# Kernel optimization log

Measured on AMD Instinct MI355X. Metric: run time of the kernel, lower is better.

Reference implementation:

```python
import jax, jax.numpy as jnp
import numpy as np

B, T, D = 4, 1024, 2048
H = 32
HD = D // H  # 64
NEG = -1e9


def setup_inputs() -> dict:
    key = jax.random.key(0)
    ks = jax.random.split(key, 12)
    s = 0.02
    x = jax.random.normal(ks[0], (B, T, D), dtype=jnp.float32)
    # additive causal mask [1, 1, T, T]
    causal = jnp.tril(jnp.ones((T, T), dtype=bool))
    attention_mask = jnp.where(causal, 0.0, NEG).astype(jnp.float32)[None, None]
    cache = jnp.zeros((B, 2, T, H, HD), dtype=jnp.float32)
    return {
        "x": x,
        "attention_mask": attention_mask,
        "cache": cache,
        "cache_update_index": 0,
        "Wq": jax.random.normal(ks[1], (D, D), jnp.float32) * s,
        "bq": jnp.zeros((D,), jnp.float32),
        "Wk": jax.random.normal(ks[2], (D, D), jnp.float32) * s,
        "bk": jnp.zeros((D,), jnp.float32),
        "Wv": jax.random.normal(ks[3], (D, D), jnp.float32) * s,
        "bv": jnp.zeros((D,), jnp.float32),
        "Wo": jax.random.normal(ks[4], (D, D), jnp.float32) * s,
        "bo": jnp.zeros((D,), jnp.float32),
    }


def _split_heads(t):
    b, s, _ = t.shape
    return t.reshape(b, s, H, HD).transpose(0, 2, 1, 3)  # (B,H,T,HD)


def reference(x, attention_mask, cache, cache_update_index, Wq, bq, Wk, bk, Wv, bv, Wo, bo):
    q = _split_heads(x @ Wq + bq)  # (B,H,T,HD)
    k = _split_heads(x @ Wk + bk)
    v = _split_heads(x @ Wv + bv)

    # update KV cache (cache layout: [B, 2, max_len, H, HD])
    k_for_cache = k.transpose(0, 2, 1, 3)  # (B,T,H,HD)
    v_for_cache = v.transpose(0, 2, 1, 3)
    idx = (0, cache_update_index, 0, 0)
    k_cache = jax.lax.dynamic_update_slice(cache[:, 0], k_for_cache, idx)
    v_cache = jax.lax.dynamic_update_slice(cache[:, 1], v_for_cache, idx)
    new_cache = jnp.stack([k_cache, v_cache], axis=1)
    k = k_cache.transpose(0, 2, 1, 3)  # (B,H,S,HD)
    v = v_cache.transpose(0, 2, 1, 3)

    scale = jnp.asarray(HD, q.dtype) ** -0.5
    scores = jnp.einsum("bhqd,bhkd->bhqk", q, k) * scale + attention_mask.astype(q.dtype)
    attn = jax.nn.softmax(scores, axis=-1)
    ctx = jnp.einsum("bhqk,bhkd->bhqd", attn, v)  # (B,H,T,HD)
    merged = ctx.transpose(0, 2, 1, 3).reshape(x.shape[0], x.shape[1], D)
    out = merged @ Wo + bo
    return out, new_cache
```

## Files before the change

### kernel.cpp

```cpp
#include <hip/hip_runtime.h>
#include <hip/hip_bf16.h>
#include <stdint.h>


typedef __hip_bfloat16 bf16;
typedef unsigned short us;
typedef short s16x8 __attribute__((ext_vector_type(8)));
typedef float f32x4 __attribute__((ext_vector_type(4)));

#define T_SEQ   1024
#define D_MODEL 2048

__device__ inline us f2b(float f) {
    bf16 h = __float2bfloat16(f);
    return *(us*)&h;
}

typedef __attribute__((address_space(1))) const void gas_void;
typedef __attribute__((address_space(3))) void las_void;

__device__ inline void gl2lds16(const void* g, void* l) {
    __builtin_amdgcn_global_load_lds((gas_void*)g, (las_void*)l, 16, 0, 0);
}

__global__ __launch_bounds__(256)
void cvtx_kernel(const float* __restrict__ x, us* __restrict__ xb)
{
    const size_t i = ((size_t)blockIdx.x * 256 + threadIdx.x) * 8;
    float4 a = *(const float4*)(x + i);
    float4 b = *(const float4*)(x + i + 4);
    union { uint4 u; us s[8]; } p;
    p.s[0] = f2b(a.x); p.s[1] = f2b(a.y); p.s[2] = f2b(a.z); p.s[3] = f2b(a.w);
    p.s[4] = f2b(b.x); p.s[5] = f2b(b.y); p.s[6] = f2b(b.z); p.s[7] = f2b(b.w);
    *(uint4*)(xb + i) = p.u;
}

__global__ __launch_bounds__(256)
void wtrans_kernel(const float* __restrict__ W0, const float* __restrict__ W1,
                   const float* __restrict__ W2, us* __restrict__ Wt)
{
    __shared__ float tile[64][65];
    const int z = blockIdx.z;
    const float* W = (z == 0) ? W0 : (z == 1) ? W1 : W2;
    us* dst = Wt + (size_t)z * D_MODEL * D_MODEL;

    const int tid = threadIdx.x;
    const int k0 = blockIdx.y * 64, n0 = blockIdx.x * 64;

    const int rr = tid >> 4, cc = (tid & 15) * 4;
    #pragma unroll
    for (int i = 0; i < 4; ++i) {
        float4 v = *(const float4*)(W + (size_t)(k0 + rr + i * 16) * D_MODEL + n0 + cc);
        tile[rr + i * 16][cc]     = v.x;
        tile[rr + i * 16][cc + 1] = v.y;
        tile[rr + i * 16][cc + 2] = v.z;
        tile[rr + i * 16][cc + 3] = v.w;
    }
    __syncthreads();

    const int nr = tid >> 3, kc = (tid & 7) * 8;
    #pragma unroll
    for (int i = 0; i < 2; ++i) {
        const int n = nr + i * 32;
        union { uint4 u; us s[8]; } p;
        #pragma unroll
        for (int j = 0; j < 8; ++j) p.s[j] = f2b(tile[kc + j][n]);
        *(uint4*)(dst + (size_t)(n0 + n) * D_MODEL + k0 + kc) = p.u;
    }
}

template<int MODE>
__global__ __launch_bounds__(256, 3)
void gemm128_kernel(const us* __restrict__ A, const us* __restrict__ Bt,
                    const float* __restrict__ b0, const float* __restrict__ b1,
                    const float* __restrict__ b2,
                    float* __restrict__ out0, float* __restrict__ out1,
                    const int* __restrict__ idxp)
{
    __shared__ __align__(16) us As[128 * 64];
    __shared__ __align__(16) us Bs[128 * 64];

    const int tid  = threadIdx.x;
    const int wv   = tid >> 6;
    const int lane = tid & 63;
    const int quad = lane >> 4;
    const int l15  = lane & 15;
    const int wm   = wv >> 1;
    const int wn   = wv & 1;

    const int gx  = gridDim.x;
    const int nwg = gx * gridDim.y;
    int bid = blockIdx.y * gx + blockIdx.x;
    bid = (bid & 7) * (nwg >> 3) + (bid >> 3);
    const int m0 = (bid / gx) * 128;
    const int n0 = (bid % gx) * 128;

    const int srow = lane >> 3;
    const int scol = ((lane & 7) ^ srow) * 8;
    const us* aG = A  + (size_t)(m0 + wv * 32 + srow) * D_MODEL + scol;
    const us* bG = Bt + (size_t)(n0 + wv * 32 + srow) * D_MODEL + scol;
    us* aL = As + wv * 32 * 64;
    us* bL = Bs + wv * 32 * 64;

    f32x4 acc[4][4];
    #pragma unroll
    for (int mi = 0; mi < 4; ++mi)
        #pragma unroll
        for (int ni = 0; ni < 4; ++ni) acc[mi][ni] = f32x4{0.f, 0.f, 0.f, 0.f};

    const int xr = l15 & 7;
    #define LDA(MI, KK) (*(const s16x8*)(As + (wm * 64 + (MI) * 16 + l15) * 64 \
                          + ((((KK) * 4 + quad) ^ xr) * 8)))
    #define LDB(NI, KK) (*(const s16x8*)(Bs + (wn * 64 + (NI) * 16 + l15) * 64 \
                          + ((((KK) * 4 + quad) ^ xr) * 8)))

    for (int k0 = 0; k0 < D_MODEL; k0 += 64) {
        #pragma unroll
        for (int g = 0; g < 4; ++g) {
            gl2lds16(aG + k0 + g * 8 * D_MODEL, aL + g * 512);
            gl2lds16(bG + k0 + g * 8 * D_MODEL, bL + g * 512);
        }
        __syncthreads();

        #pragma unroll
        for (int kk = 0; kk < 2; ++kk) {
            s16x8 af[4], bfr[4];
            #pragma unroll
            for (int mi = 0; mi < 4; ++mi) af[mi] = LDA(mi, kk);
            #pragma unroll
            for (int ni = 0; ni < 4; ++ni) bfr[ni] = LDB(ni, kk);
            #pragma unroll
            for (int mi = 0; mi < 4; ++mi)
                #pragma unroll
                for (int ni = 0; ni < 4; ++ni)
                    acc[mi][ni] = __builtin_amdgcn_mfma_f32_16x16x32_bf16(
                        af[mi], bfr[ni], acc[mi][ni], 0, 0, 0);
        }
        __syncthreads();
    }
    #undef LDA
    #undef LDB

    const int seg = (MODE == 3) ? (n0 >> 11) : 0;
    const float* bias = (MODE == 3) ? (seg == 0 ? b0 : (seg == 1 ? b1 : b2)) : b0;
    const int idx = (MODE == 3 && seg > 0) ? idxp[0] : 0;

    #pragma unroll
    for (int ni = 0; ni < 4; ++ni) {
        const int col = n0 + wn * 64 + ni * 16 + l15;
        const int cl  = col & (D_MODEL - 1);
        const float bv = bias[cl];
        #pragma unroll
        for (int mi = 0; mi < 4; ++mi) {
            #pragma unroll
            for (int r = 0; r < 4; ++r) {
                const int m = m0 + wm * 64 + mi * 16 + quad * 4 + r;
                const float v = acc[mi][ni][r] + bv;
                if (MODE == 0) {
                    out0[(size_t)m * D_MODEL + cl] = v;
                } else {
                    if (seg == 0) {
                        ((us*)out0)[(size_t)m * D_MODEL + cl] = f2b(v * 0.125f);
                    } else {
                        const int b  = m >> 10;
                        const int tt = ((m & 1023) + idx) & 1023;
                        out1[((size_t)(b * 2 + (seg - 1)) * T_SEQ + tt) * D_MODEL + cl] = v;
                    }
                }
            }
        }
    }
}

#define LDW  72
#define LDWV 70

__global__ __launch_bounds__(512, 4)
void attn_mfma_kernel(const us* __restrict__ q, const float* __restrict__ cache,
                      us* __restrict__ ctx)
{
    __shared__ __align__(16) us Qs[128 * LDW];
    __shared__ __align__(16) us Ks[64 * LDW];
    __shared__ __align__(16) us Vt[64 * LDWV];

    const int tid  = threadIdx.x;
    const int wave = tid >> 6;
    const int lane = tid & 63;
    const int quad = lane >> 4;
    const int l15  = lane & 15;

    const int bh = blockIdx.x;
    const int b  = bh >> 5;
    const int h  = bh & 31;
    const int qt = 7 - blockIdx.y;

    const float* kbase = cache + ((size_t)(b * 2 + 0) * T_SEQ) * D_MODEL + h * 64;
    const float* vbase = cache + ((size_t)(b * 2 + 1) * T_SEQ) * D_MODEL + h * 64;

    {
        const int qrow = tid >> 2;
        const int qp   = tid & 3;
        const uint4* qg = (const uint4*)(q + (size_t)(b * T_SEQ + qt * 128 + qrow) * D_MODEL
                                           + h * 64 + qp * 16);
        uint4 q0 = qg[0], q1 = qg[1];
        *(uint4*)(Qs + qrow * LDW + qp * 16)     = q0;
        *(uint4*)(Qs + qrow * LDW + qp * 16 + 8) = q1;
    }
    __syncthreads();

    const s16x8 qf0 = *(const s16x8*)(Qs + (wave * 16 + l15) * LDW + quad * 8);
    const s16x8 qf1 = *(const s16x8*)(Qs + (wave * 16 + l15) * LDW + 32 + quad * 8);

    f32x4 oacc[4];
    #pragma unroll
    for (int t = 0; t < 4; ++t) oacc[t] = f32x4{0.f, 0.f, 0.f, 0.f};
    float m_run[4] = {-1e30f, -1e30f, -1e30f, -1e30f};
    float l_run[4] = {0.f, 0.f, 0.f, 0.f};

    const int nkt = 2 * qt + 2;

    const int ksrow = tid >> 3;
    const int kp8   = tid & 7;
    const int vs    = tid >> 4;
    const int vp4   = tid & 15;

    for (int kt = 0; kt < nkt; ++kt) {
        __syncthreads();

        {
            const float4* kg = (const float4*)(kbase + (size_t)(kt * 64 + ksrow) * D_MODEL + kp8 * 8);
            float4 k0 = kg[0], k1 = kg[1];
            union { uint4 u; us s[8]; } p;
            p.s[0] = f2b(k0.x); p.s[1] = f2b(k0.y); p.s[2] = f2b(k0.z); p.s[3] = f2b(k0.w);
            p.s[4] = f2b(k1.x); p.s[5] = f2b(k1.y); p.s[6] = f2b(k1.z); p.s[7] = f2b(k1.w);
            *(uint4*)(Ks + ksrow * LDW + kp8 * 8) = p.u;
        }
        {
            const float4 a = *(const float4*)(vbase + (size_t)(kt * 64 + 2 * vs) * D_MODEL + vp4 * 4);
            const float4 c = *(const float4*)(vbase + (size_t)(kt * 64 + 2 * vs + 1) * D_MODEL + vp4 * 4);
            const float av[4] = {a.x, a.y, a.z, a.w};
            const float cv[4] = {c.x, c.y, c.z, c.w};
            #pragma unroll
            for (int j = 0; j < 4; ++j) {
                ushort2 w; w.x = f2b(av[j]); w.y = f2b(cv[j]);
                *(ushort2*)(Vt + (vp4 * 4 + j) * LDWV + 2 * vs) = w;
            }
        }
        __syncthreads();

        const int kbr = kt * 64 - qt * 128;
        if (kbr < wave * 16 + 16) {
            f32x4 sacc[4];
            #pragma unroll
            for (int t = 0; t < 4; ++t) sacc[t] = f32x4{0.f, 0.f, 0.f, 0.f};
            #pragma unroll
            for (int t = 0; t < 4; ++t) {
                s16x8 kf0 = *(const s16x8*)(Ks + (t * 16 + l15) * LDW + quad * 8);
                s16x8 kf1 = *(const s16x8*)(Ks + (t * 16 + l15) * LDW + 32 + quad * 8);
                sacc[t] = __builtin_amdgcn_mfma_f32_16x16x32_bf16(qf0, kf0, sacc[t], 0, 0, 0);
                sacc[t] = __builtin_amdgcn_mfma_f32_16x16x32_bf16(qf1, kf1, sacc[t], 0, 0, 0);
            }

            if (kbr + 63 > wave * 16) {
                #pragma unroll
                for (int t = 0; t < 4; ++t) {
                    const int keyl = kbr + t * 16 + l15;
                    #pragma unroll
                    for (int r = 0; r < 4; ++r) {
                        if (keyl > wave * 16 + quad * 4 + r) sacc[t][r] = -1e30f;
                    }
                }
            }

            float rmax[4];
            #pragma unroll
            for (int r = 0; r < 4; ++r)
                rmax[r] = fmaxf(fmaxf(sacc[0][r], sacc[1][r]), fmaxf(sacc[2][r], sacc[3][r]));
            #pragma unroll
            for (int off = 1; off < 16; off <<= 1) {
                #pragma unroll
                for (int r = 0; r < 4; ++r) rmax[r] = fmaxf(rmax[r], __shfl_xor(rmax[r], off, 16));
            }
            float alpha[4];
            #pragma unroll
            for (int r = 0; r < 4; ++r) {
                const float mnew = fmaxf(m_run[r], rmax[r]);
                alpha[r] = __expf(m_run[r] - mnew);
                m_run[r] = mnew;
            }
            float rsum[4] = {0.f, 0.f, 0.f, 0.f};
            #pragma unroll
            for (int t = 0; t < 4; ++t) {
                #pragma unroll
                for (int r = 0; r < 4; ++r) {
                    const float p = __expf(sacc[t][r] - m_run[r]);
                    sacc[t][r] = p;
                    rsum[r] += p;
                }
            }
            #pragma unroll
            for (int off = 1; off < 16; off <<= 1) {
                #pragma unroll
                for (int r = 0; r < 4; ++r) rsum[r] += __shfl_xor(rsum[r], off, 16);
            }
            #pragma unroll
            for (int r = 0; r < 4; ++r) l_run[r] = l_run[r] * alpha[r] + rsum[r];
            #pragma unroll
            for (int t = 0; t < 4; ++t) {
                #pragma unroll
                for (int r = 0; r < 4; ++r) oacc[t][r] *= alpha[r];
            }

            #pragma unroll
            for (int t = 0; t < 4; ++t) {
                #pragma unroll
                for (int r = 0; r < 4; ++r)
                    Qs[(wave * 16 + quad * 4 + r) * LDW + t * 16 + l15] = f2b(sacc[t][r]);
            }

            s16x8 pf0 = *(const s16x8*)(Qs + (wave * 16 + l15) * LDW + quad * 8);
            s16x8 pf1 = *(const s16x8*)(Qs + (wave * 16 + l15) * LDW + 32 + quad * 8);
            #pragma unroll
            for (int t = 0; t < 4; ++t) {
                s16x8 vf0 = *(const s16x8*)(Vt + (t * 16 + l15) * LDWV + quad * 8);
                s16x8 vf1 = *(const s16x8*)(Vt + (t * 16 + l15) * LDWV + 32 + quad * 8);
                oacc[t] = __builtin_amdgcn_mfma_f32_16x16x32_bf16(pf0, vf0, oacc[t], 0, 0, 0);
                oacc[t] = __builtin_amdgcn_mfma_f32_16x16x32_bf16(pf1, vf1, oacc[t], 0, 0, 0);
            }
        }
    }

    float invl[4];
    #pragma unroll
    for (int r = 0; r < 4; ++r) invl[r] = 1.0f / l_run[r];
    #pragma unroll
    for (int r = 0; r < 4; ++r) {
        const int qrow = qt * 128 + wave * 16 + quad * 4 + r;
        us* orow = ctx + (size_t)(b * T_SEQ + qrow) * D_MODEL + h * 64;
        #pragma unroll
        for (int t = 0; t < 4; ++t) orow[t * 16 + l15] = f2b(oacc[t][r] * invl[r]);
    }
}

extern "C" void kernel_launch(void* const* d_in, const int* in_sizes, int n_in,
                              void* d_out, int out_size, void* d_ws, size_t ws_size,
                              hipStream_t stream)
{
    const float* x    = (const float*)d_in[0];
    const int*   idxp = (const int*)d_in[3];
    const float* Wq   = (const float*)d_in[4];
    const float* bq   = (const float*)d_in[5];
    const float* Wk   = (const float*)d_in[6];
    const float* bk   = (const float*)d_in[7];
    const float* Wv   = (const float*)d_in[8];
    const float* bv   = (const float*)d_in[9];
    const float* Wo   = (const float*)d_in[10];
    const float* bo   = (const float*)d_in[11];

    float* out      = (float*)d_out;
    us*    xb       = (us*)d_out;
    us*    qb       = (us*)d_out + (size_t)8 * 1024 * 1024;
    float* cacheOut = out + (size_t)4 * T_SEQ * D_MODEL;

    us* WT3  = (us*)d_ws;
    us* WTo  = (us*)d_ws;
    us* ctxb = (us*)d_ws + (size_t)4 * 1024 * 1024;

    const dim3 tb(256);

    cvtx_kernel<<<dim3(4096), tb, 0, stream>>>(x, xb);
    wtrans_kernel<<<dim3(32, 32, 3), tb, 0, stream>>>(Wq, Wk, Wv, WT3);

    gemm128_kernel<3><<<dim3(48, 32), tb, 0, stream>>>(
        xb, WT3, bq, bk, bv, (float*)qb, cacheOut, idxp);

    wtrans_kernel<<<dim3(32, 32, 1), tb, 0, stream>>>(Wo, Wo, Wo, WTo);

    attn_mfma_kernel<<<dim3(128, 8), dim3(512), 0, stream>>>(qb, cacheOut, ctxb);

    gemm128_kernel<0><<<dim3(16, 32), tb, 0, stream>>>(
        ctxb, WTo, bo, nullptr, nullptr, out, nullptr, nullptr);
}
```

Measured before the change: 439.0 us.

## Split V projection to emit pre-transposed bf16 V and double-buffer attention K/V tiles

```diff
diff --git a/kernel.cpp b/kernel.cpp
--- a/kernel.cpp
+++ b/kernel.cpp
@@ -37,11 +37,11 @@
 
 __global__ __launch_bounds__(256)
 void wtrans_kernel(const float* __restrict__ W0, const float* __restrict__ W1,
-                   const float* __restrict__ W2, us* __restrict__ Wt)
+                   us* __restrict__ Wt)
 {
     __shared__ float tile[64][65];
     const int z = blockIdx.z;
-    const float* W = (z == 0) ? W0 : (z == 1) ? W1 : W2;
+    const float* W = (z == 0) ? W0 : W1;
     us* dst = Wt + (size_t)z * D_MODEL * D_MODEL;
 
     const int tid = threadIdx.x;
@@ -73,9 +73,8 @@
 __global__ __launch_bounds__(256, 3)
 void gemm128_kernel(const us* __restrict__ A, const us* __restrict__ Bt,
                     const float* __restrict__ b0, const float* __restrict__ b1,
-                    const float* __restrict__ b2,
                     float* __restrict__ out0, float* __restrict__ out1,
-                    const int* __restrict__ idxp)
+                    us* __restrict__ vbt, const int* __restrict__ idxp)
 {
     __shared__ __align__(16) us As[128 * 64];
     __shared__ __align__(16) us Bs[128 * 64];
@@ -141,9 +140,9 @@
     #undef LDA
     #undef LDB
 
-    const int seg = (MODE == 3) ? (n0 >> 11) : 0;
-    const float* bias = (MODE == 3) ? (seg == 0 ? b0 : (seg == 1 ? b1 : b2)) : b0;
-    const int idx = (MODE == 3 && seg > 0) ? idxp[0] : 0;
+    const int seg = (MODE == 4) ? (n0 >> 11) : 0;
+    const float* bias = (MODE == 4) ? (seg == 0 ? b0 : b1) : b0;
+    const int idx = (MODE == 0) ? 0 : idxp[0];
 
     #pragma unroll
     for (int ni = 0; ni < 4; ++ni) {
@@ -152,42 +151,57 @@
         const float bv = bias[cl];
         #pragma unroll
         for (int mi = 0; mi < 4; ++mi) {
+            float vv[4];
             #pragma unroll
             for (int r = 0; r < 4; ++r) {
                 const int m = m0 + wm * 64 + mi * 16 + quad * 4 + r;
                 const float v = acc[mi][ni][r] + bv;
                 if (MODE == 0) {
                     out0[(size_t)m * D_MODEL + cl] = v;
-                } else {
+                } else if (MODE == 4) {
                     if (seg == 0) {
                         ((us*)out0)[(size_t)m * D_MODEL + cl] = f2b(v * 0.125f);
                     } else {
                         const int b  = m >> 10;
                         const int tt = ((m & 1023) + idx) & 1023;
-                        out1[((size_t)(b * 2 + (seg - 1)) * T_SEQ + tt) * D_MODEL + cl] = v;
+                        out1[((size_t)(b * 2 + 0) * T_SEQ + tt) * D_MODEL + cl] = v;
                     }
+                } else {
+                    const int b  = m >> 10;
+                    const int tt = ((m & 1023) + idx) & 1023;
+                    out1[((size_t)(b * 2 + 1) * T_SEQ + tt) * D_MODEL + cl] = v;
+                    vv[r] = v;
                 }
             }
-        }
-    }
-}
-
-#define LDW  72
-#define LDWV 70
+            if (MODE == 5) {
+                const int tok0 = m0 + wm * 64 + mi * 16 + quad * 4;
+                const int bb = tok0 >> 10, t0 = tok0 & 1023;
+                const int hh = cl >> 6, dd = cl & 63;
+                ushort4 pv;
+                pv.x = f2b(vv[0]); pv.y = f2b(vv[1]);
+                pv.z = f2b(vv[2]); pv.w = f2b(vv[3]);
+                *(ushort4*)(vbt + (size_t)((bb * 32 + hh) * 64 + dd) * 1024 + t0) = pv;
+            }
+        }
+    }
+}
+
+#define LDW 72
 
 __global__ __launch_bounds__(512, 4)
 void attn_mfma_kernel(const us* __restrict__ q, const float* __restrict__ cache,
-                      us* __restrict__ ctx)
+                      const us* __restrict__ vbt, us* __restrict__ ctx)
 {
     __shared__ __align__(16) us Qs[128 * LDW];
-    __shared__ __align__(16) us Ks[64 * LDW];
-    __shared__ __align__(16) us Vt[64 * LDWV];
+    __shared__ __align__(16) us Ks[2][64 * LDW];
+    __shared__ __align__(16) us Vt[2][64 * 64];
 
     const int tid  = threadIdx.x;
     const int wave = tid >> 6;
     const int lane = tid & 63;
     const int quad = lane >> 4;
     const int l15  = lane & 15;
+    const int xr   = l15 & 7;
 
     const int bh = blockIdx.x;
     const int b  = bh >> 5;
@@ -195,7 +209,7 @@
     const int qt = 7 - blockIdx.y;
 
     const float* kbase = cache + ((size_t)(b * 2 + 0) * T_SEQ) * D_MODEL + h * 64;
-    const float* vbase = cache + ((size_t)(b * 2 + 1) * T_SEQ) * D_MODEL + h * 64;
+    const us* vb_bh = vbt + (size_t)((b * 32 + h) * 64) * 1024;
 
     {
         const int qrow = tid >> 2;
@@ -206,6 +220,24 @@
         *(uint4*)(Qs + qrow * LDW + qp * 16)     = q0;
         *(uint4*)(Qs + qrow * LDW + qp * 16 + 8) = q1;
     }
+
+    const int ksrow = tid >> 3;
+    const int kp8   = tid & 7;
+    const int vrow  = lane >> 3;
+    const int vchk  = (lane & 7) ^ vrow;
+    const us* vG = vb_bh + (size_t)(wave * 8 + vrow) * 1024 + vchk * 8;
+
+    const int nkt = 2 * qt + 2;
+
+    gl2lds16(vG, (us*)Vt[0] + wave * 512);
+    {
+        const float4* kg = (const float4*)(kbase + (size_t)ksrow * D_MODEL + kp8 * 8);
+        float4 k0 = kg[0], k1 = kg[1];
+        union { uint4 u; us s[8]; } p;
+        p.s[0] = f2b(k0.x); p.s[1] = f2b(k0.y); p.s[2] = f2b(k0.z); p.s[3] = f2b(k0.w);
+        p.s[4] = f2b(k1.x); p.s[5] = f2b(k1.y); p.s[6] = f2b(k1.z); p.s[7] = f2b(k1.w);
+        *(uint4*)(&Ks[0][ksrow * LDW + kp8 * 8]) = p.u;
+    }
     __syncthreads();
 
     const s16x8 qf0 = *(const s16x8*)(Qs + (wave * 16 + l15) * LDW + quad * 8);
@@ -217,46 +249,30 @@
     float m_run[4] = {-1e30f, -1e30f, -1e30f, -1e30f};
     float l_run[4] = {0.f, 0.f, 0.f, 0.f};
 
-    const int nkt = 2 * qt + 2;
-
-    const int ksrow = tid >> 3;
-    const int kp8   = tid & 7;
-    const int vs    = tid >> 4;
-    const int vp4   = tid & 15;
-
     for (int kt = 0; kt < nkt; ++kt) {
-        __syncthreads();
-
-        {
-            const float4* kg = (const float4*)(kbase + (size_t)(kt * 64 + ksrow) * D_MODEL + kp8 * 8);
-            float4 k0 = kg[0], k1 = kg[1];
-            union { uint4 u; us s[8]; } p;
-            p.s[0] = f2b(k0.x); p.s[1] = f2b(k0.y); p.s[2] = f2b(k0.z); p.s[3] = f2b(k0.w);
-            p.s[4] = f2b(k1.x); p.s[5] = f2b(k1.y); p.s[6] = f2b(k1.z); p.s[7] = f2b(k1.w);
-            *(uint4*)(Ks + ksrow * LDW + kp8 * 8) = p.u;
-        }
-        {
-            const float4 a = *(const float4*)(vbase + (size_t)(kt * 64 + 2 * vs) * D_MODEL + vp4 * 4);
-            const float4 c = *(const float4*)(vbase + (size_t)(kt * 64 + 2 * vs + 1) * D_MODEL + vp4 * 4);
-            const float av[4] = {a.x, a.y, a.z, a.w};
-            const float cv[4] = {c.x, c.y, c.z, c.w};
-            #pragma unroll
-            for (int j = 0; j < 4; ++j) {
-                ushort2 w; w.x = f2b(av[j]); w.y = f2b(cv[j]);
-                *(ushort2*)(Vt + (vp4 * 4 + j) * LDWV + 2 * vs) = w;
-            }
-        }
-        __syncthreads();
+        const int buf = kt & 1;
+        const bool more = (kt + 1 < nkt);
+
+        float4 nk0, nk1;
+        if (more) {
+            gl2lds16(vG + (kt + 1) * 64, (us*)Vt[buf ^ 1] + wave * 512);
+            const float4* kg = (const float4*)(kbase
+                + (size_t)((kt + 1) * 64 + ksrow) * D_MODEL + kp8 * 8);
+            nk0 = kg[0]; nk1 = kg[1];
+        }
 
         const int kbr = kt * 64 - qt * 128;
         if (kbr < wave * 16 + 16) {
+            const us* kb_ = Ks[buf];
+            const us* vb_ = (const us*)Vt[buf];
+
             f32x4 sacc[4];
             #pragma unroll
             for (int t = 0; t < 4; ++t) sacc[t] = f32x4{0.f, 0.f, 0.f, 0.f};
             #pragma unroll
             for (int t = 0; t < 4; ++t) {
-                s16x8 kf0 = *(const s16x8*)(Ks + (t * 16 + l15) * LDW + quad * 8);
-                s16x8 kf1 = *(const s16x8*)(Ks + (t * 16 + l15) * LDW + 32 + quad * 8);
+                s16x8 kf0 = *(const s16x8*)(kb_ + (t * 16 + l15) * LDW + quad * 8);
+                s16x8 kf1 = *(const s16x8*)(kb_ + (t * 16 + l15) * LDW + 32 + quad * 8);
                 sacc[t] = __builtin_amdgcn_mfma_f32_16x16x32_bf16(qf0, kf0, sacc[t], 0, 0, 0);
                 sacc[t] = __builtin_amdgcn_mfma_f32_16x16x32_bf16(qf1, kf1, sacc[t], 0, 0, 0);
             }
@@ -322,12 +338,20 @@
             s16x8 pf1 = *(const s16x8*)(Qs + (wave * 16 + l15) * LDW + 32 + quad * 8);
             #pragma unroll
             for (int t = 0; t < 4; ++t) {
-                s16x8 vf0 = *(const s16x8*)(Vt + (t * 16 + l15) * LDWV + quad * 8);
-                s16x8 vf1 = *(const s16x8*)(Vt + (t * 16 + l15) * LDWV + 32 + quad * 8);
+                s16x8 vf0 = *(const s16x8*)(vb_ + (t * 16 + l15) * 64 + ((quad ^ xr) * 8));
+                s16x8 vf1 = *(const s16x8*)(vb_ + (t * 16 + l15) * 64 + (((4 + quad) ^ xr) * 8));
                 oacc[t] = __builtin_amdgcn_mfma_f32_16x16x32_bf16(pf0, vf0, oacc[t], 0, 0, 0);
                 oacc[t] = __builtin_amdgcn_mfma_f32_16x16x32_bf16(pf1, vf1, oacc[t], 0, 0, 0);
             }
         }
+
+        if (more) {
+            union { uint4 u; us s[8]; } p;
+            p.s[0] = f2b(nk0.x); p.s[1] = f2b(nk0.y); p.s[2] = f2b(nk0.z); p.s[3] = f2b(nk0.w);
+            p.s[4] = f2b(nk1.x); p.s[5] = f2b(nk1.y); p.s[6] = f2b(nk1.z); p.s[7] = f2b(nk1.w);
+            *(uint4*)(&Ks[buf ^ 1][ksrow * LDW + kp8 * 8]) = p.u;
+        }
+        __syncthreads();
     }
 
     float invl[4];
@@ -362,22 +386,29 @@
     us*    qb       = (us*)d_out + (size_t)8 * 1024 * 1024;
     float* cacheOut = out + (size_t)4 * T_SEQ * D_MODEL;
 
-    us* WT3  = (us*)d_ws;
+    us* WTqk = (us*)d_ws;
+    us* WTv  = (us*)d_ws + (size_t)8 * 1024 * 1024;
+    us* vbt  = (us*)d_ws;
+    us* ctxb = (us*)d_ws + (size_t)8 * 1024 * 1024;
     us* WTo  = (us*)d_ws;
-    us* ctxb = (us*)d_ws + (size_t)4 * 1024 * 1024;
 
     const dim3 tb(256);
 
     cvtx_kernel<<<dim3(4096), tb, 0, stream>>>(x, xb);
-    wtrans_kernel<<<dim3(32, 32, 3), tb, 0, stream>>>(Wq, Wk, Wv, WT3);
-
-    gemm128_kernel<3><<<dim3(48, 32), tb, 0, stream>>>(
-        xb, WT3, bq, bk, bv, (float*)qb, cacheOut, idxp);
-
-    wtrans_kernel<<<dim3(32, 32, 1), tb, 0, stream>>>(Wo, Wo, Wo, WTo);
-
-    attn_mfma_kernel<<<dim3(128, 8), dim3(512), 0, stream>>>(qb, cacheOut, ctxb);
+    wtrans_kernel<<<dim3(32, 32, 2), tb, 0, stream>>>(Wq, Wk, WTqk);
+
+    gemm128_kernel<4><<<dim3(32, 32), tb, 0, stream>>>(
+        xb, WTqk, bq, bk, (float*)qb, cacheOut, nullptr, idxp);
+
+    wtrans_kernel<<<dim3(32, 32, 1), tb, 0, stream>>>(Wv, Wv, WTv);
+
+    gemm128_kernel<5><<<dim3(16, 32), tb, 0, stream>>>(
+        xb, WTv, bv, nullptr, nullptr, cacheOut, vbt, idxp);
+
+    attn_mfma_kernel<<<dim3(128, 8), dim3(512), 0, stream>>>(qb, cacheOut, vbt, ctxb);
+
+    wtrans_kernel<<<dim3(32, 32, 1), tb, 0, stream>>>(Wo, Wo, WTo);
 
     gemm128_kernel<0><<<dim3(16, 32), tb, 0, stream>>>(
-        ctxb, WTo, bo, nullptr, nullptr, out, nullptr, nullptr);
-}
+        ctxb, WTo, bo, nullptr, out, nullptr, nullptr, nullptr);
+}
```

New measurement: 441.6 us. About the same (+0.6%).
